# Performance work log

Hardware: AMD Instinct MI355X
Metric: run time of the kernel (lower is better)

The kernel has to match this reference:

```python
import jax, jax.numpy as jnp
import numpy as np


def _seq_shifts(n, max_len):
    # alternating-sign powers of two: [1,-1,2,-2,4,-4,...] capped by max_len
    shifts = []
    i = 0
    while len(shifts) < n and 2 ** i < max_len:
        shifts.append(2 ** i)
        if len(shifts) < n:
            shifts.append(-(2 ** i))
        i += 1
    return shifts

SPATIAL_SHIFTS = _seq_shifts(12, 2048)   # [1,-1,2,-2,4,-4,8,-8,16,-16,32,-32]
TEMPORAL_SHIFTS = _seq_shifts(4, 1 << 30)  # [1,-1,2,-2]
EPS = 1e-6


def setup_inputs() -> dict:
    key = jax.random.key(0)
    ks = jax.random.split(key, 8)
    B, L, C, H, D = 1, 8192, 1024, 16, 64
    inner = H * D
    w = 1.0 / np.sqrt(C)
    x = jax.random.normal(ks[0], (B, L, C), jnp.float32)
    Wq = jax.random.normal(ks[1], (C, inner), jnp.float32) * w
    Wk = jax.random.normal(ks[2], (C, inner), jnp.float32) * w
    Wv = jax.random.normal(ks[3], (C, inner), jnp.float32) * w
    Wo = jax.random.normal(ks[4], (inner, C), jnp.float32) * w
    bq = jnp.zeros((inner,), jnp.float32)
    bk = jnp.zeros((inner,), jnp.float32)
    bv = jnp.zeros((inner,), jnp.float32)
    bo = jnp.zeros((C,), jnp.float32)
    qn_w = jnp.ones((inner,), jnp.float32)
    kn_w = jnp.ones((inner,), jnp.float32)
    # edge bias initialized per the module's __init__ formula
    eb = np.zeros((H, len(SPATIAL_SHIFTS) + len(TEMPORAL_SHIFTS)), np.float32)
    for i, s in enumerate(SPATIAL_SHIFTS):
        eb[:, i] = 0.1 * np.log1p(abs(s))
    for i, s in enumerate(TEMPORAL_SHIFTS):
        eb[:, len(SPATIAL_SHIFTS) + i] = 0.2 * np.log1p(abs(s))
    edge_bias = jnp.asarray(eb)
    return {"x": x, "Wq": Wq, "bq": bq, "Wk": Wk, "bk": bk, "Wv": Wv, "bv": bv,
            "qn_w": qn_w, "kn_w": kn_w, "edge_bias": edge_bias, "Wo": Wo, "bo": bo,
            "num_frames": 8}


def _rms(t, w):
    return t * jax.lax.rsqrt(jnp.mean(t * t, axis=-1, keepdims=True) + EPS) * w


def reference(x, Wq, bq, Wk, bk, Wv, bv, qn_w, kn_w, edge_bias, Wo, bo, num_frames):
    B, L, _ = x.shape
    T = int(num_frames)
    S = L // T
    H, n_shifts = edge_bias.shape
    D = Wq.shape[1] // H
    scale = D ** -0.5
    msg = _rms(x @ Wq + bq, qn_w).reshape(B, T, S, H, D)
    key = _rms(x @ Wk + bk, kn_w).reshape(B, T, S, H, D)
    v5 = (x @ Wv + bv).reshape(B, T, S, H, D)
    scores, vals = [], []
    for s in SPATIAL_SHIFTS:  # neighbor idx (i+s)%S along spatial axis == roll(-s)
        k_nb = jnp.roll(key, -s, axis=2)
        vals.append(jnp.roll(v5, -s, axis=2))
        scores.append(jnp.einsum('btshd,btshd->btsh', msg, k_nb) * scale)
    for t in TEMPORAL_SHIFTS:  # neighbor idx (f+t)%T along frame axis
        k_nb = jnp.roll(key, -t, axis=1)
        vals.append(jnp.roll(v5, -t, axis=1))
        scores.append(jnp.einsum('btshd,btshd->btsh', msg, k_nb) * scale)
    sc = jnp.stack(scores, axis=-1) + edge_bias  # [B,T,S,H,N]
    attn = jax.nn.softmax(sc, axis=-1)
    v_stack = jnp.stack(vals, axis=-1)  # [B,T,S,H,D,N]
    out = jnp.einsum('btshn,btshdn->btshd', attn, v_stack).reshape(B, L, H * D)
    return out @ Wo + bo
```

## Files before the change

### kernel.cpp

```cpp
#include <hip/hip_runtime.h>
#include <hip/hip_bf16.h>

typedef __bf16 bf16x8 __attribute__((ext_vector_type(8)));
typedef float f32x4 __attribute__((ext_vector_type(4)));
typedef unsigned short ushort8 __attribute__((ext_vector_type(8)));
typedef unsigned short ushort_t;

#define AS3(p) ((__attribute__((address_space(3))) void*)(p))
#define AS1(p) ((const __attribute__((address_space(1))) void*)(p))

constexpr int L = 8192;
constexpr int C = 1024;
constexpr int T = 8;
constexpr int S = 1024;

__device__ __forceinline__ float bf2f(ushort_t u) {
    return __uint_as_float(((unsigned)u) << 16);
}
__device__ __forceinline__ ushort_t f2bf(float f) {
    unsigned x = __float_as_uint(f);
    unsigned r = (x + 0x7fffu + ((x >> 16) & 1u)) >> 16;
    return (ushort_t)r;
}

__global__ __launch_bounds__(256) void cvt_kernel(const float* __restrict__ in,
                                                  ushort_t* __restrict__ out, int n8) {
    int i = blockIdx.x * 256 + threadIdx.x;
    if (i >= n8) return;
    const float4* p = (const float4*)in + (long)i * 2;
    float4 a = p[0], b = p[1];
    ushort8 o;
    o[0] = f2bf(a.x); o[1] = f2bf(a.y); o[2] = f2bf(a.z); o[3] = f2bf(a.w);
    o[4] = f2bf(b.x); o[5] = f2bf(b.y); o[6] = f2bf(b.z); o[7] = f2bf(b.w);
    ((ushort8*)out)[i] = o;
}

__global__ __launch_bounds__(256) void transpose4_kernel(
    const float* __restrict__ w0, const float* __restrict__ w1,
    const float* __restrict__ w2, const float* __restrict__ w3,
    ushort_t* __restrict__ o0, ushort_t* __restrict__ o1,
    ushort_t* __restrict__ o2, ushort_t* __restrict__ o3) {
    int z = blockIdx.z;
    const float* W = z == 0 ? w0 : z == 1 ? w1 : z == 2 ? w2 : w3;
    ushort_t* O    = z == 0 ? o0 : z == 1 ? o1 : z == 2 ? o2 : o3;
    __shared__ float tile[32][33];
    int tx = threadIdx.x & 31, ty = threadIdx.x >> 5;
    int bx = blockIdx.x * 32, by = blockIdx.y * 32;
#pragma unroll
    for (int i = 0; i < 32; i += 8)
        tile[ty + i][tx] = W[(long)(by + ty + i) * C + bx + tx];
    __syncthreads();
#pragma unroll
    for (int i = 0; i < 32; i += 8)
        O[(long)(bx + ty + i) * C + by + tx] = f2bf(tile[tx][ty + i]);
}

template <bool BF16_OUT>
__device__ __forceinline__ void gemm_body(const ushort_t* __restrict__ A,
                                          const ushort_t* __restrict__ Bt,
                                          const float* __restrict__ bias,
                                          void* __restrict__ Cv,
                                          int M, int N, int K, int bx, int by) {
    __shared__ ushort_t As[128 * 32];
    __shared__ ushort_t Bs[128 * 32];

    const int tid = threadIdx.x;
    const int wave = tid >> 6, lane = tid & 63;
    const int wr = wave >> 1, wc = wave & 1;
    const int bm0 = bx * 128, bn0 = by * 128;

    f32x4 acc[4][4] = {};

    const int ci0 = tid, ci1 = tid + 256;
    const char* Ab = (const char*)A;
    const char* Bb = (const char*)Bt;
    const long aoff0 = ((long)(bm0 + (ci0 >> 2)) * K + (ci0 & 3) * 8) * 2;
    const long aoff1 = ((long)(bm0 + (ci1 >> 2)) * K + (ci1 & 3) * 8) * 2;
    const long boff0 = ((long)(bn0 + (ci0 >> 2)) * K + (ci0 & 3) * 8) * 2;
    const long boff1 = ((long)(bn0 + (ci1 >> 2)) * K + (ci1 & 3) * 8) * 2;
    char* ldsA = (char*)As;
    char* ldsB = (char*)Bs;
    const unsigned l0 = wave * 1024u;
    const unsigned l1 = 4096u + wave * 1024u;

    const int k0 = (lane >> 4) * 8;
    const int ra = wr * 64 + (lane & 15);
    const int cbn = wc * 64 + (lane & 15);

    for (int kt = 0; kt < K; kt += 32) {
        const long kb = (long)kt * 2;
        __builtin_amdgcn_global_load_lds(AS1(Ab + aoff0 + kb), AS3(ldsA + l0), 16, 0, 0);
        __builtin_amdgcn_global_load_lds(AS1(Ab + aoff1 + kb), AS3(ldsA + l1), 16, 0, 0);
        __builtin_amdgcn_global_load_lds(AS1(Bb + boff0 + kb), AS3(ldsB + l0), 16, 0, 0);
        __builtin_amdgcn_global_load_lds(AS1(Bb + boff1 + kb), AS3(ldsB + l1), 16, 0, 0);
        __syncthreads();

        bf16x8 af[4], bfr[4];
#pragma unroll
        for (int m = 0; m < 4; m++)
            af[m] = *(const bf16x8*)(As + (ra + m * 16) * 32 + k0);
#pragma unroll
        for (int n = 0; n < 4; n++)
            bfr[n] = *(const bf16x8*)(Bs + (cbn + n * 16) * 32 + k0);
#pragma unroll
        for (int m = 0; m < 4; m++)
#pragma unroll
            for (int n = 0; n < 4; n++)
                acc[m][n] = __builtin_amdgcn_mfma_f32_16x16x32_bf16(af[m], bfr[n],
                                                                    acc[m][n], 0, 0, 0);
        __syncthreads();
    }

    const int r0 = bm0 + wr * 64 + (lane >> 4) * 4;
    const int c0 = bn0 + wc * 64 + (lane & 15);
#pragma unroll
    for (int n = 0; n < 4; n++) {
        const int col = c0 + n * 16;
        const float bia = bias[col];
#pragma unroll
        for (int m = 0; m < 4; m++) {
            const int row = r0 + m * 16;
#pragma unroll
            for (int r = 0; r < 4; r++) {
                float val = acc[m][n][r] + bia;
                if (BF16_OUT)
                    ((ushort_t*)Cv)[(long)(row + r) * N + col] = f2bf(val);
                else
                    ((float*)Cv)[(long)(row + r) * N + col] = val;
            }
        }
    }
}

__global__ __launch_bounds__(256) void gemm_qkv_kernel(
    const ushort_t* __restrict__ xbf,
    const ushort_t* __restrict__ WqT, const ushort_t* __restrict__ WkT,
    const ushort_t* __restrict__ WvT,
    const float* __restrict__ bq, const float* __restrict__ bk,
    const float* __restrict__ bv,
    ushort_t* __restrict__ q, ushort_t* __restrict__ k, ushort_t* __restrict__ v) {
    const int z = blockIdx.z;
    const ushort_t* Bt = z == 0 ? WqT : z == 1 ? WkT : WvT;
    const float* bias  = z == 0 ? bq : z == 1 ? bk : bv;
    ushort_t* out      = z == 0 ? q : z == 1 ? k : v;
    gemm_body<true>(xbf, Bt, bias, out, L, C, C, blockIdx.x, blockIdx.y);
}

__global__ __launch_bounds__(256) void gemm_o_kernel(
    const ushort_t* __restrict__ a, const ushort_t* __restrict__ WoT,
    const float* __restrict__ bo, float* __restrict__ outp) {
    gemm_body<false>(a, WoT, bo, outp, L, C, C, blockIdx.x, blockIdx.y);
}

__global__ __launch_bounds__(256) void attn_kernel(
    const ushort_t* __restrict__ qraw, const ushort_t* __restrict__ kraw,
    const ushort_t* __restrict__ vraw,
    const float* __restrict__ qn_w, const float* __restrict__ kn_w,
    const float* __restrict__ eb, ushort_t* __restrict__ outp) {
    const int wave = threadIdx.x >> 6, lane = threadIdx.x & 63;
    const int p = blockIdx.x * 4 + wave;
    const int t = p >> 10, s = p & (S - 1);
    const int h = lane >> 2;
    const int cb = lane * 16;

    float qf[16];
    {
        const ushort8* qp = (const ushort8*)(qraw + (long)p * C + cb);
        ushort8 a = qp[0], b = qp[1];
#pragma unroll
        for (int j = 0; j < 8; j++) { qf[j] = bf2f(a[j]); qf[8 + j] = bf2f(b[j]); }
    }
    float ss = 0.f;
#pragma unroll
    for (int j = 0; j < 16; j++) ss += qf[j] * qf[j];
#pragma unroll
    for (int m = 1; m < 64; m <<= 1) ss += __shfl_xor(ss, m);
    const float rq = rsqrtf(ss * (1.0f / C) + 1e-6f);
#pragma unroll
    for (int j = 0; j < 16; j++) qf[j] *= rq * qn_w[cb + j] * kn_w[cb + j];

    const int SHF[16] = {1, -1, 2, -2, 4, -4, 8, -8, 16, -16, 32, -32, 1, -1, 2, -2};
    int pp[16];
#pragma unroll
    for (int n = 0; n < 16; n++) {
        if (n < 12) pp[n] = (p & ~(S - 1)) | ((s + SHF[n]) & (S - 1));
        else        pp[n] = (((t + SHF[n]) & (T - 1)) << 10) | s;
    }

    float sc[16];
#pragma unroll
    for (int n = 0; n < 16; n++) {
        const ushort8* kp = (const ushort8*)(kraw + (long)pp[n] * C + cb);
        ushort8 a = kp[0], b = kp[1];
        float kf[16];
#pragma unroll
        for (int j = 0; j < 8; j++) { kf[j] = bf2f(a[j]); kf[8 + j] = bf2f(b[j]); }
        float ssk = 0.f, dot = 0.f;
#pragma unroll
        for (int j = 0; j < 16; j++) { ssk += kf[j] * kf[j]; dot += qf[j] * kf[j]; }
#pragma unroll
        for (int m = 1; m < 64; m <<= 1) ssk += __shfl_xor(ssk, m);
        dot += __shfl_xor(dot, 1);
        dot += __shfl_xor(dot, 2);
        const float rk = rsqrtf(ssk * (1.0f / C) + 1e-6f);
        sc[n] = dot * rk * 0.125f + eb[h * 16 + n];
    }

    float mx = sc[0];
#pragma unroll
    for (int n = 1; n < 16; n++) mx = fmaxf(mx, sc[n]);
    float wts[16], den = 0.f;
#pragma unroll
    for (int n = 0; n < 16; n++) { wts[n] = __expf(sc[n] - mx); den += wts[n]; }
    const float inv = 1.0f / den;

    float o[16] = {};
#pragma unroll
    for (int n = 0; n < 16; n++) {
        const ushort8* vp = (const ushort8*)(vraw + (long)pp[n] * C + cb);
        ushort8 a = vp[0], b = vp[1];
#pragma unroll
        for (int j = 0; j < 8; j++) {
            o[j]     += wts[n] * bf2f(a[j]);
            o[8 + j] += wts[n] * bf2f(b[j]);
        }
    }

    ushort8 oa, ob;
#pragma unroll
    for (int j = 0; j < 8; j++) { oa[j] = f2bf(o[j] * inv); ob[j] = f2bf(o[8 + j] * inv); }
    ushort8* op = (ushort8*)(outp + (long)p * C + cb);
    op[0] = oa;
    op[1] = ob;
}

extern "C" void kernel_launch(void* const* d_in, const int* in_sizes, int n_in,
                              void* d_out, int out_size, void* d_ws, size_t ws_size,
                              hipStream_t stream) {
    const float* x    = (const float*)d_in[0];
    const float* Wq   = (const float*)d_in[1];
    const float* bq   = (const float*)d_in[2];
    const float* Wk   = (const float*)d_in[3];
    const float* bk   = (const float*)d_in[4];
    const float* Wv   = (const float*)d_in[5];
    const float* bv   = (const float*)d_in[6];
    const float* qn_w = (const float*)d_in[7];
    const float* kn_w = (const float*)d_in[8];
    const float* eb   = (const float*)d_in[9];
    const float* Wo   = (const float*)d_in[10];
    const float* bo   = (const float*)d_in[11];

    char* ws = (char*)d_ws;
    ushort_t* xbf  = (ushort_t*)ws;
    ushort_t* WqT  = (ushort_t*)(ws + (size_t)L * C * 2);
    ushort_t* WkT  = WqT + (size_t)C * C;
    ushort_t* WvT  = WkT + (size_t)C * C;
    ushort_t* WoT  = WvT + (size_t)C * C;
    ushort_t* qraw = WoT + (size_t)C * C;
    ushort_t* kraw = qraw + (size_t)L * C;
    ushort_t* vraw = kraw + (size_t)L * C;
    ushort_t* aout = vraw + (size_t)L * C;
    float* outp = (float*)d_out;

    cvt_kernel<<<(L * C / 8 + 255) / 256, 256, 0, stream>>>(x, xbf, L * C / 8);
    transpose4_kernel<<<dim3(32, 32, 4), 256, 0, stream>>>(Wq, Wk, Wv, Wo,
                                                           WqT, WkT, WvT, WoT);
    gemm_qkv_kernel<<<dim3(L / 128, C / 128, 3), 256, 0, stream>>>(
        xbf, WqT, WkT, WvT, bq, bk, bv, qraw, kraw, vraw);
    attn_kernel<<<L / 4, 256, 0, stream>>>(qraw, kraw, vraw, qn_w, kn_w, eb, aout);
    gemm_o_kernel<<<dim3(L / 128, C / 128), 256, 0, stream>>>(aout, WoT, bo, outp);
}
```

Measured before the change: 247.7 us.

## Rewrite GEMMs as 8-wave triple-buffered swizzled kernels and precompute RMS norms

```diff
diff --git a/kernel.cpp b/kernel.cpp
--- a/kernel.cpp
+++ b/kernel.cpp
@@ -55,70 +55,142 @@
         O[(long)(bx + ty + i) * C + by + tx] = f2bf(tile[tx][ty + i]);
 }
 
+constexpr int BUFB = 49152;
+
+#define GBAR() asm volatile("s_barrier" ::: "memory")
+#define VMBAR6() asm volatile("s_waitcnt vmcnt(6)\ns_barrier" ::: "memory")
+#define VMBAR0() asm volatile("s_waitcnt vmcnt(0)\ns_barrier" ::: "memory")
+
 template <bool BF16_OUT>
-__device__ __forceinline__ void gemm_body(const ushort_t* __restrict__ A,
-                                          const ushort_t* __restrict__ Bt,
-                                          const float* __restrict__ bias,
-                                          void* __restrict__ Cv,
-                                          int M, int N, int K, int bx, int by) {
-    __shared__ ushort_t As[128 * 32];
-    __shared__ ushort_t Bs[128 * 32];
-
+__device__ __forceinline__ void gemm8_body(const ushort_t* __restrict__ A,
+                                           const ushort_t* __restrict__ Bt,
+                                           const float* __restrict__ bias,
+                                           void* __restrict__ Cv,
+                                           int M, int N, int K, int bx, int by) {
+    __shared__ char lds[3 * BUFB];
     const int tid = threadIdx.x;
     const int wave = tid >> 6, lane = tid & 63;
-    const int wr = wave >> 1, wc = wave & 1;
-    const int bm0 = bx * 128, bn0 = by * 128;
-
-    f32x4 acc[4][4] = {};
-
-    const int ci0 = tid, ci1 = tid + 256;
+    const int wm = wave >> 2, wn = wave & 3;
+    const int bm0 = bx * 256, bn0 = by * 128;
+    const int KT = K >> 6;
+
     const char* Ab = (const char*)A;
     const char* Bb = (const char*)Bt;
-    const long aoff0 = ((long)(bm0 + (ci0 >> 2)) * K + (ci0 & 3) * 8) * 2;
-    const long aoff1 = ((long)(bm0 + (ci1 >> 2)) * K + (ci1 & 3) * 8) * 2;
-    const long boff0 = ((long)(bn0 + (ci0 >> 2)) * K + (ci0 & 3) * 8) * 2;
-    const long boff1 = ((long)(bn0 + (ci1 >> 2)) * K + (ci1 & 3) * 8) * 2;
-    char* ldsA = (char*)As;
-    char* ldsB = (char*)Bs;
-    const unsigned l0 = wave * 1024u;
-    const unsigned l1 = 4096u + wave * 1024u;
-
-    const int k0 = (lane >> 4) * 8;
-    const int ra = wr * 64 + (lane & 15);
-    const int cbn = wc * 64 + (lane & 15);
-
-    for (int kt = 0; kt < K; kt += 32) {
-        const long kb = (long)kt * 2;
-        __builtin_amdgcn_global_load_lds(AS1(Ab + aoff0 + kb), AS3(ldsA + l0), 16, 0, 0);
-        __builtin_amdgcn_global_load_lds(AS1(Ab + aoff1 + kb), AS3(ldsA + l1), 16, 0, 0);
-        __builtin_amdgcn_global_load_lds(AS1(Bb + boff0 + kb), AS3(ldsB + l0), 16, 0, 0);
-        __builtin_amdgcn_global_load_lds(AS1(Bb + boff1 + kb), AS3(ldsB + l1), 16, 0, 0);
-        __syncthreads();
-
-        bf16x8 af[4], bfr[4];
-#pragma unroll
-        for (int m = 0; m < 4; m++)
-            af[m] = *(const bf16x8*)(As + (ra + m * 16) * 32 + k0);
-#pragma unroll
-        for (int n = 0; n < 4; n++)
-            bfr[n] = *(const bf16x8*)(Bs + (cbn + n * 16) * 32 + k0);
-#pragma unroll
-        for (int m = 0; m < 4; m++)
-#pragma unroll
-            for (int n = 0; n < 4; n++)
-                acc[m][n] = __builtin_amdgcn_mfma_f32_16x16x32_bf16(af[m], bfr[n],
-                                                                    acc[m][n], 0, 0, 0);
-        __syncthreads();
-    }
-
-    const int r0 = bm0 + wr * 64 + (lane >> 4) * 4;
-    const int c0 = bn0 + wc * 64 + (lane & 15);
-#pragma unroll
-    for (int n = 0; n < 4; n++) {
+    long aSrc[4], bSrc[2];
+#pragma unroll
+    for (int j = 0; j < 4; j++) {
+        int c = tid + j * 512, row = c >> 3, scol = (c & 7) ^ (row & 7);
+        aSrc[j] = ((long)(bm0 + row) * K + scol * 8) * 2;
+    }
+#pragma unroll
+    for (int j = 0; j < 2; j++) {
+        int c = tid + j * 512, row = c >> 3, scol = (c & 7) ^ (row & 7);
+        bSrc[j] = ((long)(bn0 + row) * K + scol * 8) * 2;
+    }
+    const unsigned wOff = wave * 1024u;
+
+#define STAGE_A(it2, cb, j) \
+    __builtin_amdgcn_global_load_lds(AS1(Ab + aSrc[j] + (long)(it2) * 128), \
+        AS3(lds + (cb) * BUFB + (j) * 8192 + wOff), 16, 0, 0)
+#define STAGE_B(it2, cb, j) \
+    __builtin_amdgcn_global_load_lds(AS1(Bb + bSrc[j] + (long)(it2) * 128), \
+        AS3(lds + (cb) * BUFB + 32768 + (j) * 8192 + wOff), 16, 0, 0)
+
+    const unsigned cs0 = (((lane >> 4)) ^ (lane & 7)) * 16u;
+    const unsigned cs1 = (((lane >> 4) + 4) ^ (lane & 7)) * 16u;
+    const unsigned rA = (wm * 128 + (lane & 15)) * 128u;
+    const unsigned rB = (wn * 32 + (lane & 15)) * 128u;
+
+    f32x4 acc[8][2] = {};
+    bf16x8 af[4][2], bf0[2], bf1[2];
+
+#pragma unroll
+    for (int j = 0; j < 4; j++) STAGE_A(0, 0, j);
+#pragma unroll
+    for (int j = 0; j < 2; j++) STAGE_B(0, 0, j);
+#pragma unroll
+    for (int j = 0; j < 4; j++) STAGE_A(1, 1, j);
+#pragma unroll
+    for (int j = 0; j < 2; j++) STAGE_B(1, 1, j);
+    VMBAR6();
+
+    int c = 0;
+    for (int it = 0; it < KT; ++it) {
+        const char* bA = lds + c * BUFB;
+        const char* bB = bA + 32768;
+        const int c2 = (c == 0) ? 2 : c - 1;
+        const int it2 = it + 2;
+        const bool stage = it2 < KT;
+
+#pragma unroll
+        for (int q = 0; q < 4; q++) {
+            af[q][0] = *(const bf16x8*)(bA + rA + q * 2048 + cs0);
+            af[q][1] = *(const bf16x8*)(bA + rA + q * 2048 + cs1);
+        }
+        bf0[0] = *(const bf16x8*)(bB + rB + cs0);
+        bf0[1] = *(const bf16x8*)(bB + rB + cs1);
+        if (stage) { STAGE_A(it2, c2, 0); STAGE_A(it2, c2, 1); }
+        GBAR();
+        __builtin_amdgcn_s_setprio(1);
+#pragma unroll
+        for (int q = 0; q < 4; q++) {
+            acc[q][0] = __builtin_amdgcn_mfma_f32_16x16x32_bf16(af[q][0], bf0[0], acc[q][0], 0, 0, 0);
+            acc[q][0] = __builtin_amdgcn_mfma_f32_16x16x32_bf16(af[q][1], bf0[1], acc[q][0], 0, 0, 0);
+        }
+        __builtin_amdgcn_s_setprio(0);
+        GBAR();
+
+        bf1[0] = *(const bf16x8*)(bB + rB + 2048 + cs0);
+        bf1[1] = *(const bf16x8*)(bB + rB + 2048 + cs1);
+        if (stage) { STAGE_A(it2, c2, 2); STAGE_A(it2, c2, 3); }
+        GBAR();
+        __builtin_amdgcn_s_setprio(1);
+#pragma unroll
+        for (int q = 0; q < 4; q++) {
+            acc[q][1] = __builtin_amdgcn_mfma_f32_16x16x32_bf16(af[q][0], bf1[0], acc[q][1], 0, 0, 0);
+            acc[q][1] = __builtin_amdgcn_mfma_f32_16x16x32_bf16(af[q][1], bf1[1], acc[q][1], 0, 0, 0);
+        }
+        __builtin_amdgcn_s_setprio(0);
+        GBAR();
+
+#pragma unroll
+        for (int q = 0; q < 4; q++) {
+            af[q][0] = *(const bf16x8*)(bA + rA + (4 + q) * 2048 + cs0);
+            af[q][1] = *(const bf16x8*)(bA + rA + (4 + q) * 2048 + cs1);
+        }
+        if (stage) { STAGE_B(it2, c2, 0); STAGE_B(it2, c2, 1); }
+        GBAR();
+        __builtin_amdgcn_s_setprio(1);
+#pragma unroll
+        for (int q = 0; q < 4; q++) {
+            acc[4 + q][0] = __builtin_amdgcn_mfma_f32_16x16x32_bf16(af[q][0], bf0[0], acc[4 + q][0], 0, 0, 0);
+            acc[4 + q][0] = __builtin_amdgcn_mfma_f32_16x16x32_bf16(af[q][1], bf0[1], acc[4 + q][0], 0, 0, 0);
+        }
+        __builtin_amdgcn_s_setprio(0);
+        GBAR();
+
+        __builtin_amdgcn_s_setprio(1);
+#pragma unroll
+        for (int q = 0; q < 4; q++) {
+            acc[4 + q][1] = __builtin_amdgcn_mfma_f32_16x16x32_bf16(af[q][0], bf1[0], acc[4 + q][1], 0, 0, 0);
+            acc[4 + q][1] = __builtin_amdgcn_mfma_f32_16x16x32_bf16(af[q][1], bf1[1], acc[4 + q][1], 0, 0, 0);
+        }
+        __builtin_amdgcn_s_setprio(0);
+
+        if (it < KT - 1) {
+            if (stage) VMBAR6(); else VMBAR0();
+        }
+        c = (c == 2) ? 0 : c + 1;
+    }
+
+    const int r0 = bm0 + wm * 128 + (lane >> 4) * 4;
+    const int c0 = bn0 + wn * 32 + (lane & 15);
+#pragma unroll
+    for (int n = 0; n < 2; n++) {
         const int col = c0 + n * 16;
         const float bia = bias[col];
 #pragma unroll
-        for (int m = 0; m < 4; m++) {
+        for (int m = 0; m < 8; m++) {
             const int row = r0 + m * 16;
 #pragma unroll
             for (int r = 0; r < 4; r++) {
@@ -130,9 +202,11 @@
             }
         }
     }
-}
-
-__global__ __launch_bounds__(256) void gemm_qkv_kernel(
+#undef STAGE_A
+#undef STAGE_B
+}
+
+__global__ __launch_bounds__(512) void gemm_qkv_kernel(
     const ushort_t* __restrict__ xbf,
     const ushort_t* __restrict__ WqT, const ushort_t* __restrict__ WkT,
     const ushort_t* __restrict__ WvT,
@@ -143,23 +217,50 @@
     const ushort_t* Bt = z == 0 ? WqT : z == 1 ? WkT : WvT;
     const float* bias  = z == 0 ? bq : z == 1 ? bk : bv;
     ushort_t* out      = z == 0 ? q : z == 1 ? k : v;
-    gemm_body<true>(xbf, Bt, bias, out, L, C, C, blockIdx.x, blockIdx.y);
-}
-
-__global__ __launch_bounds__(256) void gemm_o_kernel(
+    gemm8_body<true>(xbf, Bt, bias, out, L, C, C, blockIdx.x, blockIdx.y);
+}
+
+__global__ __launch_bounds__(512) void gemm_o_kernel(
     const ushort_t* __restrict__ a, const ushort_t* __restrict__ WoT,
     const float* __restrict__ bo, float* __restrict__ outp) {
-    gemm_body<false>(a, WoT, bo, outp, L, C, C, blockIdx.x, blockIdx.y);
+    gemm8_body<false>(a, WoT, bo, outp, L, C, C, blockIdx.x, blockIdx.y);
+}
+
+__global__ __launch_bounds__(256) void rownorm_kernel(
+    const ushort_t* __restrict__ q, const ushort_t* __restrict__ k,
+    float* __restrict__ rq, float* __restrict__ rk) {
+    const int wave = threadIdx.x >> 6, lane = threadIdx.x & 63;
+    const int p = blockIdx.x * 4 + wave;
+    const ushort8* qp = (const ushort8*)(q + (long)p * C + lane * 16);
+    const ushort8* kp = (const ushort8*)(k + (long)p * C + lane * 16);
+    ushort8 qa = qp[0], qb = qp[1], ka = kp[0], kb = kp[1];
+    float sq = 0.f, sk = 0.f;
+#pragma unroll
+    for (int j = 0; j < 8; j++) {
+        float a = bf2f(qa[j]), b = bf2f(qb[j]);
+        sq += a * a + b * b;
+        float c2 = bf2f(ka[j]), d = bf2f(kb[j]);
+        sk += c2 * c2 + d * d;
+    }
+#pragma unroll
+    for (int m = 1; m < 64; m <<= 1) { sq += __shfl_xor(sq, m); sk += __shfl_xor(sk, m); }
+    if (lane == 0) {
+        rq[p] = rsqrtf(sq * (1.0f / C) + 1e-6f);
+        rk[p] = rsqrtf(sk * (1.0f / C) + 1e-6f);
+    }
 }
 
 __global__ __launch_bounds__(256) void attn_kernel(
     const ushort_t* __restrict__ qraw, const ushort_t* __restrict__ kraw,
     const ushort_t* __restrict__ vraw,
     const float* __restrict__ qn_w, const float* __restrict__ kn_w,
-    const float* __restrict__ eb, ushort_t* __restrict__ outp) {
+    const float* __restrict__ eb, const float* __restrict__ rqA,
+    const float* __restrict__ rkA, ushort_t* __restrict__ outp) {
     const int wave = threadIdx.x >> 6, lane = threadIdx.x & 63;
-    const int p = blockIdx.x * 4 + wave;
-    const int t = p >> 10, s = p & (S - 1);
+    const int bid = blockIdx.x;
+    const int t = bid & 7;
+    const int s = (bid >> 3) * 4 + wave;
+    const int p = (t << 10) | s;
     const int h = lane >> 2;
     const int cb = lane * 16;
 
@@ -170,12 +271,7 @@
 #pragma unroll
         for (int j = 0; j < 8; j++) { qf[j] = bf2f(a[j]); qf[8 + j] = bf2f(b[j]); }
     }
-    float ss = 0.f;
-#pragma unroll
-    for (int j = 0; j < 16; j++) ss += qf[j] * qf[j];
-#pragma unroll
-    for (int m = 1; m < 64; m <<= 1) ss += __shfl_xor(ss, m);
-    const float rq = rsqrtf(ss * (1.0f / C) + 1e-6f);
+    const float rq = rqA[p];
 #pragma unroll
     for (int j = 0; j < 16; j++) qf[j] *= rq * qn_w[cb + j] * kn_w[cb + j];
 
@@ -192,18 +288,12 @@
     for (int n = 0; n < 16; n++) {
         const ushort8* kp = (const ushort8*)(kraw + (long)pp[n] * C + cb);
         ushort8 a = kp[0], b = kp[1];
-        float kf[16];
-#pragma unroll
-        for (int j = 0; j < 8; j++) { kf[j] = bf2f(a[j]); kf[8 + j] = bf2f(b[j]); }
-        float ssk = 0.f, dot = 0.f;
-#pragma unroll
-        for (int j = 0; j < 16; j++) { ssk += kf[j] * kf[j]; dot += qf[j] * kf[j]; }
-#pragma unroll
-        for (int m = 1; m < 64; m <<= 1) ssk += __shfl_xor(ssk, m);
+        float dot = 0.f;
+#pragma unroll
+        for (int j = 0; j < 8; j++) dot += qf[j] * bf2f(a[j]) + qf[8 + j] * bf2f(b[j]);
         dot += __shfl_xor(dot, 1);
         dot += __shfl_xor(dot, 2);
-        const float rk = rsqrtf(ssk * (1.0f / C) + 1e-6f);
-        sc[n] = dot * rk * 0.125f + eb[h * 16 + n];
+        sc[n] = dot * (rkA[pp[n]] * 0.125f) + eb[h * 16 + n];
     }
 
     float mx = sc[0];
@@ -260,13 +350,17 @@
     ushort_t* kraw = qraw + (size_t)L * C;
     ushort_t* vraw = kraw + (size_t)L * C;
     ushort_t* aout = vraw + (size_t)L * C;
+    float* rqArr   = (float*)(aout + (size_t)L * C);
+    float* rkArr   = rqArr + L;
     float* outp = (float*)d_out;
 
     cvt_kernel<<<(L * C / 8 + 255) / 256, 256, 0, stream>>>(x, xbf, L * C / 8);
     transpose4_kernel<<<dim3(32, 32, 4), 256, 0, stream>>>(Wq, Wk, Wv, Wo,
                                                            WqT, WkT, WvT, WoT);
-    gemm_qkv_kernel<<<dim3(L / 128, C / 128, 3), 256, 0, stream>>>(
+    gemm_qkv_kernel<<<dim3(L / 256, C / 128, 3), 512, 0, stream>>>(
         xbf, WqT, WkT, WvT, bq, bk, bv, qraw, kraw, vraw);
-    attn_kernel<<<L / 4, 256, 0, stream>>>(qraw, kraw, vraw, qn_w, kn_w, eb, aout);
-    gemm_o_kernel<<<dim3(L / 128, C / 128), 256, 0, stream>>>(aout, WoT, bo, outp);
-}
+    rownorm_kernel<<<L / 4, 256, 0, stream>>>(qraw, kraw, rqArr, rkArr);
+    attn_kernel<<<L / 4, 256, 0, stream>>>(qraw, kraw, vraw, qn_w, kn_w, eb,
+                                           rqArr, rkArr, aout);
+    gemm_o_kernel<<<dim3(L / 256, C / 128), 512, 0, stream>>>(aout, WoT, bo, outp);
+}
```

Measured after the change: 241.0 us. 2.7% less time.

## Triple-buffer GEMM with 256x128 tiles, precompute key norms, reorder attention blocks

Applied to the files above, without the earlier changes.

```diff
diff --git a/kernel.cpp b/kernel.cpp
--- a/kernel.cpp
+++ b/kernel.cpp
@@ -55,74 +55,98 @@
         O[(long)(bx + ty + i) * C + by + tx] = f2bf(tile[tx][ty + i]);
 }
 
+#define VMBAR6() asm volatile("s_waitcnt vmcnt(6)\ns_barrier" ::: "memory")
+#define VMBAR0() asm volatile("s_waitcnt vmcnt(0)\ns_barrier" ::: "memory")
+
 template <bool BF16_OUT>
 __device__ __forceinline__ void gemm_body(const ushort_t* __restrict__ A,
                                           const ushort_t* __restrict__ Bt,
                                           const float* __restrict__ bias,
                                           void* __restrict__ Cv,
-                                          int M, int N, int K, int bx, int by) {
-    __shared__ ushort_t As[128 * 32];
-    __shared__ ushort_t Bs[128 * 32];
-
+                                          int K, int N, int bx, int by) {
+    __shared__ char lds[3 * 24576];
     const int tid = threadIdx.x;
     const int wave = tid >> 6, lane = tid & 63;
-    const int wr = wave >> 1, wc = wave & 1;
-    const int bm0 = bx * 128, bn0 = by * 128;
-
-    f32x4 acc[4][4] = {};
-
-    const int ci0 = tid, ci1 = tid + 256;
+    const int wm = wave >> 1, wn = wave & 1;
+    const long bm0 = (long)bx * 256, bn0 = (long)by * 128;
+    const int KT = K >> 5;
+
     const char* Ab = (const char*)A;
     const char* Bb = (const char*)Bt;
-    const long aoff0 = ((long)(bm0 + (ci0 >> 2)) * K + (ci0 & 3) * 8) * 2;
-    const long aoff1 = ((long)(bm0 + (ci1 >> 2)) * K + (ci1 & 3) * 8) * 2;
-    const long boff0 = ((long)(bn0 + (ci0 >> 2)) * K + (ci0 & 3) * 8) * 2;
-    const long boff1 = ((long)(bn0 + (ci1 >> 2)) * K + (ci1 & 3) * 8) * 2;
-    char* ldsA = (char*)As;
-    char* ldsB = (char*)Bs;
-    const unsigned l0 = wave * 1024u;
-    const unsigned l1 = 4096u + wave * 1024u;
-
-    const int k0 = (lane >> 4) * 8;
-    const int ra = wr * 64 + (lane & 15);
-    const int cbn = wc * 64 + (lane & 15);
-
-    for (int kt = 0; kt < K; kt += 32) {
-        const long kb = (long)kt * 2;
-        __builtin_amdgcn_global_load_lds(AS1(Ab + aoff0 + kb), AS3(ldsA + l0), 16, 0, 0);
-        __builtin_amdgcn_global_load_lds(AS1(Ab + aoff1 + kb), AS3(ldsA + l1), 16, 0, 0);
-        __builtin_amdgcn_global_load_lds(AS1(Bb + boff0 + kb), AS3(ldsB + l0), 16, 0, 0);
-        __builtin_amdgcn_global_load_lds(AS1(Bb + boff1 + kb), AS3(ldsB + l1), 16, 0, 0);
-        __syncthreads();
-
-        bf16x8 af[4], bfr[4];
-#pragma unroll
-        for (int m = 0; m < 4; m++)
-            af[m] = *(const bf16x8*)(As + (ra + m * 16) * 32 + k0);
-#pragma unroll
-        for (int n = 0; n < 4; n++)
-            bfr[n] = *(const bf16x8*)(Bs + (cbn + n * 16) * 32 + k0);
-#pragma unroll
-        for (int m = 0; m < 4; m++)
-#pragma unroll
-            for (int n = 0; n < 4; n++)
-                acc[m][n] = __builtin_amdgcn_mfma_f32_16x16x32_bf16(af[m], bfr[n],
-                                                                    acc[m][n], 0, 0, 0);
-        __syncthreads();
-    }
-
-    const int r0 = bm0 + wr * 64 + (lane >> 4) * 4;
-    const int c0 = bn0 + wc * 64 + (lane & 15);
-#pragma unroll
-    for (int n = 0; n < 4; n++) {
-        const int col = c0 + n * 16;
+    long aSrc[4], bSrc[2];
+#pragma unroll
+    for (int j = 0; j < 4; j++) {
+        int cc = tid + j * 256;
+        aSrc[j] = (bm0 + (cc >> 2)) * (long)(K * 2) + (cc & 3) * 16;
+    }
+#pragma unroll
+    for (int j = 0; j < 2; j++) {
+        int cc = tid + j * 256;
+        bSrc[j] = (bn0 + (cc >> 2)) * (long)(K * 2) + (cc & 3) * 16;
+    }
+    const unsigned wOff = wave * 1024u;
+
+#define STG(buf, it2)                                                          \
+    do {                                                                       \
+        const long kb_ = (long)(it2) * 64;                                     \
+        char* bs_ = lds + (buf) * 24576;                                       \
+        _Pragma("unroll") for (int j = 0; j < 4; j++)                          \
+            __builtin_amdgcn_global_load_lds(AS1(Ab + aSrc[j] + kb_),          \
+                AS3(bs_ + j * 4096 + wOff), 16, 0, 0);                         \
+        _Pragma("unroll") for (int j = 0; j < 2; j++)                          \
+            __builtin_amdgcn_global_load_lds(AS1(Bb + bSrc[j] + kb_),          \
+                AS3(bs_ + 16384 + j * 4096 + wOff), 16, 0, 0);                 \
+    } while (0)
+
+    const unsigned rdA = (wm * 128 + (lane & 15)) * 64u + (lane >> 4) * 16u;
+    const unsigned rdB = 16384u + (wn * 64 + (lane & 15)) * 64u + (lane >> 4) * 16u;
+
+    f32x4 acc[8][4] = {};
+
+    STG(0, 0);
+    STG(1, 1);
+    VMBAR6();
+
+    int c = 0;
+    for (int it = 0; it < KT; ++it) {
+        const int c2 = (c >= 1) ? c - 1 : 2;
+        if (it + 2 < KT) STG(c2, it + 2);
+
+        const char* bs = lds + c * 24576;
+        bf16x8 af[8], bfr[4];
+#pragma unroll
+        for (int q = 0; q < 8; q++)
+            af[q] = *(const bf16x8*)(bs + rdA + q * 1024);
+#pragma unroll
+        for (int j = 0; j < 4; j++)
+            bfr[j] = *(const bf16x8*)(bs + rdB + j * 1024);
+
+        __builtin_amdgcn_s_setprio(1);
+#pragma unroll
+        for (int q = 0; q < 8; q++)
+#pragma unroll
+            for (int j = 0; j < 4; j++)
+                acc[q][j] = __builtin_amdgcn_mfma_f32_16x16x32_bf16(af[q], bfr[j],
+                                                                    acc[q][j], 0, 0, 0);
+        __builtin_amdgcn_s_setprio(0);
+
+        if (it + 2 < KT)      VMBAR6();
+        else if (it + 1 < KT) VMBAR0();
+        c = (c >= 2) ? 0 : c + 1;
+    }
+
+    const int r0 = (int)bm0 + wm * 128 + (lane >> 4) * 4;
+    const int c0 = (int)bn0 + wn * 64 + (lane & 15);
+#pragma unroll
+    for (int j = 0; j < 4; j++) {
+        const int col = c0 + j * 16;
         const float bia = bias[col];
 #pragma unroll
-        for (int m = 0; m < 4; m++) {
-            const int row = r0 + m * 16;
+        for (int q = 0; q < 8; q++) {
+            const int row = r0 + q * 16;
 #pragma unroll
             for (int r = 0; r < 4; r++) {
-                float val = acc[m][n][r] + bia;
+                float val = acc[q][j][r] + bia;
                 if (BF16_OUT)
                     ((ushort_t*)Cv)[(long)(row + r) * N + col] = f2bf(val);
                 else
@@ -130,9 +154,10 @@
             }
         }
     }
-}
-
-__global__ __launch_bounds__(256) void gemm_qkv_kernel(
+#undef STG
+}
+
+__global__ __launch_bounds__(256, 2) void gemm_qkv_kernel(
     const ushort_t* __restrict__ xbf,
     const ushort_t* __restrict__ WqT, const ushort_t* __restrict__ WkT,
     const ushort_t* __restrict__ WvT,
@@ -143,23 +168,43 @@
     const ushort_t* Bt = z == 0 ? WqT : z == 1 ? WkT : WvT;
     const float* bias  = z == 0 ? bq : z == 1 ? bk : bv;
     ushort_t* out      = z == 0 ? q : z == 1 ? k : v;
-    gemm_body<true>(xbf, Bt, bias, out, L, C, C, blockIdx.x, blockIdx.y);
-}
-
-__global__ __launch_bounds__(256) void gemm_o_kernel(
+    gemm_body<true>(xbf, Bt, bias, out, C, C, blockIdx.x, blockIdx.y);
+}
+
+__global__ __launch_bounds__(256, 2) void gemm_o_kernel(
     const ushort_t* __restrict__ a, const ushort_t* __restrict__ WoT,
     const float* __restrict__ bo, float* __restrict__ outp) {
-    gemm_body<false>(a, WoT, bo, outp, L, C, C, blockIdx.x, blockIdx.y);
+    gemm_body<false>(a, WoT, bo, outp, C, C, blockIdx.x, blockIdx.y);
+}
+
+__global__ __launch_bounds__(256) void rownorm_k_kernel(
+    const ushort_t* __restrict__ k, float* __restrict__ rk) {
+    const int wave = threadIdx.x >> 6, lane = threadIdx.x & 63;
+    const int p = blockIdx.x * 4 + wave;
+    const ushort8* kp = (const ushort8*)(k + (long)p * C + lane * 16);
+    ushort8 ka = kp[0], kb = kp[1];
+    float sk = 0.f;
+#pragma unroll
+    for (int j = 0; j < 8; j++) {
+        float c2 = bf2f(ka[j]), d = bf2f(kb[j]);
+        sk += c2 * c2 + d * d;
+    }
+#pragma unroll
+    for (int m = 1; m < 64; m <<= 1) sk += __shfl_xor(sk, m);
+    if (lane == 0) rk[p] = rsqrtf(sk * (1.0f / C) + 1e-6f);
 }
 
 __global__ __launch_bounds__(256) void attn_kernel(
     const ushort_t* __restrict__ qraw, const ushort_t* __restrict__ kraw,
     const ushort_t* __restrict__ vraw,
     const float* __restrict__ qn_w, const float* __restrict__ kn_w,
-    const float* __restrict__ eb, ushort_t* __restrict__ outp) {
+    const float* __restrict__ eb, const float* __restrict__ rkA,
+    ushort_t* __restrict__ outp) {
     const int wave = threadIdx.x >> 6, lane = threadIdx.x & 63;
-    const int p = blockIdx.x * 4 + wave;
-    const int t = p >> 10, s = p & (S - 1);
+    const int bid = blockIdx.x;
+    const int t = bid & 7;
+    const int s = (bid >> 3) * 4 + wave;
+    const int p = (t << 10) | s;
     const int h = lane >> 2;
     const int cb = lane * 16;
 
@@ -192,18 +237,12 @@
     for (int n = 0; n < 16; n++) {
         const ushort8* kp = (const ushort8*)(kraw + (long)pp[n] * C + cb);
         ushort8 a = kp[0], b = kp[1];
-        float kf[16];
-#pragma unroll
-        for (int j = 0; j < 8; j++) { kf[j] = bf2f(a[j]); kf[8 + j] = bf2f(b[j]); }
-        float ssk = 0.f, dot = 0.f;
-#pragma unroll
-        for (int j = 0; j < 16; j++) { ssk += kf[j] * kf[j]; dot += qf[j] * kf[j]; }
-#pragma unroll
-        for (int m = 1; m < 64; m <<= 1) ssk += __shfl_xor(ssk, m);
+        float dot = 0.f;
+#pragma unroll
+        for (int j = 0; j < 8; j++) dot += qf[j] * bf2f(a[j]) + qf[8 + j] * bf2f(b[j]);
         dot += __shfl_xor(dot, 1);
         dot += __shfl_xor(dot, 2);
-        const float rk = rsqrtf(ssk * (1.0f / C) + 1e-6f);
-        sc[n] = dot * rk * 0.125f + eb[h * 16 + n];
+        sc[n] = dot * (rkA[pp[n]] * 0.125f) + eb[h * 16 + n];
     }
 
     float mx = sc[0];
@@ -260,13 +299,16 @@
     ushort_t* kraw = qraw + (size_t)L * C;
     ushort_t* vraw = kraw + (size_t)L * C;
     ushort_t* aout = vraw + (size_t)L * C;
+    float* rkArr   = (float*)(aout + (size_t)L * C);
     float* outp = (float*)d_out;
 
     cvt_kernel<<<(L * C / 8 + 255) / 256, 256, 0, stream>>>(x, xbf, L * C / 8);
     transpose4_kernel<<<dim3(32, 32, 4), 256, 0, stream>>>(Wq, Wk, Wv, Wo,
                                                            WqT, WkT, WvT, WoT);
-    gemm_qkv_kernel<<<dim3(L / 128, C / 128, 3), 256, 0, stream>>>(
+    gemm_qkv_kernel<<<dim3(L / 256, C / 128, 3), 256, 0, stream>>>(
         xbf, WqT, WkT, WvT, bq, bk, bv, qraw, kraw, vraw);
-    attn_kernel<<<L / 4, 256, 0, stream>>>(qraw, kraw, vraw, qn_w, kn_w, eb, aout);
-    gemm_o_kernel<<<dim3(L / 128, C / 128), 256, 0, stream>>>(aout, WoT, bo, outp);
-}
+    rownorm_k_kernel<<<L / 4, 256, 0, stream>>>(kraw, rkArr);
+    attn_kernel<<<L / 4, 256, 0, stream>>>(qraw, kraw, vraw, qn_w, kn_w, eb,
+                                           rkArr, aout);
+    gemm_o_kernel<<<dim3(L / 256, C / 128), 256, 0, stream>>>(aout, WoT, bo, outp);
+}
```

Result: faster. 237.5 us (-4.1%).
